# Kernel optimization log

Hardware: AMD Instinct MI355X
Metric: run time of the kernel (lower is better)

Reference implementation:

```python
import jax, jax.numpy as jnp
import numpy as np
import math

N = 8192
F_IN = 1024
F_OUT = 1024
MAX_ITER = 10


def whale_optimizer(positions, key, max_iter=MAX_ITER):
    """Vectorized whale optimization algorithm.

    Faithful to the original per-agent/per-dim update rules, but the agent
    loop is vectorized (on-device RNG, one parallel update per outer
    iteration); only the `max_iter` outer iterations stay sequential.
    positions: [N, D] float32.
    """
    n, d = positions.shape
    lower = jnp.min(positions)
    upper = jnp.max(positions)
    k0, loop_key = jax.random.split(key)
    leader = positions[jax.random.randint(k0, (), 0, n)]  # [D]

    def step(carry, it):
        pos, leader = carry
        itf = it.astype(jnp.float32)
        k = jax.random.fold_in(loop_key, it)
        k1, k2, k3, k4, k5, k6 = jax.random.split(k, 6)
        a = 2.0 - itf * (2.0 / max_iter)
        a2 = -1.0 + itf * (-1.0 / max_iter)
        r1 = jax.random.uniform(k1, (n, 1))
        r2 = jax.random.uniform(k2, (n, 1))
        A = 2.0 * a * r1 - a                       # [n,1]
        C = 2.0 * r2                               # [n,1]
        lp = (a2 - 1.0) * jax.random.uniform(k3, (n, 1)) + 1.0  # spiral param
        p = jax.random.uniform(k4, (n, 1))
        # random leader per (agent, dim), as in the original inner j-loop
        ridx = jax.random.randint(k5, (n, d), 0, n)
        x_rand = jnp.take_along_axis(pos, ridx, axis=0)         # [n,d]
        explore = jnp.abs(x_rand - A * jnp.abs(C * x_rand - pos))
        exploit = jnp.abs(leader - A * jnp.abs(C * leader - pos))
        spiral = jnp.abs(jnp.abs(leader - pos) * jnp.exp(lp) * jnp.cos(2.0 * jnp.pi * lp) + leader)
        new_pos = jnp.where(p < 0.5,
                            jnp.where(jnp.abs(A) >= 1.0, explore, exploit),
                            spiral)
        new_pos = jnp.clip(new_pos, lower, upper)
        new_leader = new_pos[jax.random.randint(k6, (), 0, n)]
        return (new_pos, new_leader), None

    (positions, _), _ = jax.lax.scan(step, (positions, leader), jnp.arange(max_iter))
    return positions


def setup_inputs() -> dict:
    key = jax.random.key(0)
    k1, k2, k3, k4 = jax.random.split(key, 4)
    stdv = 1.0 / math.sqrt(F_OUT)
    return {
        "input": jax.random.normal(k1, (N, F_IN), dtype=jnp.float32),
        "adj": jax.random.uniform(k2, (N, N), dtype=jnp.float32) * (1.0 / N),
        "h0": jax.random.normal(k3, (N, F_IN), dtype=jnp.float32),
        "weight": jax.random.uniform(k4, (F_IN, F_OUT), dtype=jnp.float32,
                                      minval=-stdv, maxval=stdv),
        "lamda": jnp.float32(0.5),
        "alpha": jnp.float32(0.1),
        "l": 1,
    }


def reference(input, adj, h0, weight, lamda, alpha, l):
    # variant=False, residual=False
    theta = jnp.log(lamda / l + 1.0)
    hi = adj @ input                                  # spmm(adj, input)
    support = (1.0 - alpha) * hi + alpha * h0
    r = support
    # original detaches support before the whale optimizer
    opt = whale_optimizer(jax.lax.stop_gradient(support), jax.random.key(42))
    output = theta * (opt @ weight) + (1.0 - theta) * r
    return output
```

## Files before the change

kernel.cpp:

```cpp
#include <hip/hip_runtime.h>
#include <hip/hip_bf16.h>
#include <stdint.h>
#include <math.h>

typedef uint32_t u32;
typedef __hip_bfloat16 bf16t;
typedef __attribute__((ext_vector_type(8))) short short8;
typedef __attribute__((ext_vector_type(4))) float f32x4;


__host__ __device__ __forceinline__ void tf2(u32 k0, u32 k1, u32 c0, u32 c1, u32& o0, u32& o1) {
  const u32 ks2 = k0 ^ k1 ^ 0x1BD11BDAu;
  u32 x0 = c0 + k0, x1 = c1 + k1;
#define TFROT(v,r) (((v)<<(r))|((v)>>(32-(r))))
#define TFR(r) { x0 += x1; x1 = TFROT(x1,r); x1 ^= x0; }
  TFR(13) TFR(15) TFR(26) TFR(6)   x0 += k1;  x1 += ks2 + 1u;
  TFR(17) TFR(29) TFR(16) TFR(24)  x0 += ks2; x1 += k0 + 2u;
  TFR(13) TFR(15) TFR(26) TFR(6)   x0 += k0;  x1 += k1 + 3u;
  TFR(17) TFR(29) TFR(16) TFR(24)  x0 += k1;  x1 += ks2 + 4u;
  TFR(13) TFR(15) TFR(26) TFR(6)   x0 += ks2; x1 += k0 + 5u;
#undef TFR
#undef TFROT
  o0 = x0; o1 = x1;
}

__device__ __forceinline__ float unif_row(u32 ka, u32 kb, int i) {
  u32 o0, o1;
  tf2(ka, kb, 0u, (u32)i, o0, o1);
  return __uint_as_float(0x3F800000u | ((o0 ^ o1) >> 9)) - 1.0f;
}

__device__ __forceinline__ int ridx_fn(u32 ka, u32 kb, u32 f) {
  u32 o0, o1; tf2(ka, kb, 0u, f, o0, o1); return (int)((o0 ^ o1) & 8191u);
}

static inline void split2(u32 ka, u32 kb, u32* kA, u32* kB) {
  u32 a0, a1, b0, b1;
  tf2(ka, kb, 0u, 0u, a0, a1);
  tf2(ka, kb, 0u, 1u, b0, b1);
  kA[0] = a0; kA[1] = a1; kB[0] = b0; kB[1] = b1;
}

static inline void split6(u32 ka, u32 kb, u32 out[6][2]) {
  for (u32 i = 0; i < 6; i++) { u32 o0, o1; tf2(ka, kb, 0u, i, o0, o1); out[i][0] = o0; out[i][1] = o1; }
}

static inline int scalar_randint8192(u32 ka, u32 kb) {
  u32 kA[2], kB[2];
  split2(ka, kb, kA, kB);
  u32 o0, o1;
  tf2(kB[0], kB[1], 0u, 0u, o0, o1);
  return (int)((o0 ^ o1) & 8191u);
}

__device__ __forceinline__ ushort f2bf(float f) {
  u32 u = __float_as_uint(f);
  u32 r = u + 0x7FFFu + ((u >> 16) & 1u);
  return (ushort)(r >> 16);
}

__global__ __launch_bounds__(256) void packb_k(const float* __restrict__ B, uint4* __restrict__ out, int K, int Nn) {
  const int idx = blockIdx.x * 256 + threadIdx.x;
  const int total = (K >> 3) * Nn;
  if (idx >= total) return;
  const int g = idx / Nn;
  const int n = idx - g * Nn;
  u32 wv[4];
#pragma unroll
  for (int j = 0; j < 4; j++) {
    const float f0 = B[(size_t)(g * 8 + 2 * j) * Nn + n];
    const float f1 = B[(size_t)(g * 8 + 2 * j + 1) * Nn + n];
    wv[j] = (u32)f2bf(f0) | ((u32)f2bf(f1) << 16);
  }
  uint4 o; o.x = wv[0]; o.y = wv[1]; o.z = wv[2]; o.w = wv[3];
  out[idx] = o;
}

__global__ __launch_bounds__(256) void minmax2_k(const float* __restrict__ part, int G, float* __restrict__ bnd) {
  __shared__ float slo[256], shi[256];
  const int tid = threadIdx.x;
  float lo = 3.4e38f, hi = -3.4e38f;
  for (int i = tid; i < G; i += 256) { lo = fminf(lo, part[i]); hi = fmaxf(hi, part[G + i]); }
  slo[tid] = lo; shi[tid] = hi; __syncthreads();
  for (int s = 128; s > 0; s >>= 1) {
    if (tid < s) { slo[tid] = fminf(slo[tid], slo[tid + s]); shi[tid] = fmaxf(shi[tid], shi[tid + s]); }
    __syncthreads();
  }
  if (tid == 0) { bnd[0] = slo[0]; bnd[1] = shi[0]; }
}

__device__ __forceinline__ void gld_lds16(const void* g, void* l) {
  __builtin_amdgcn_global_load_lds((const __attribute__((address_space(1))) void*)g,
                                   (__attribute__((address_space(3))) void*)l, 16, 0, 0);
}

template <int EPI, int AF32>
__global__ __launch_bounds__(512, 4) void gemm_k(
    const void* __restrict__ Araw, const bf16t* __restrict__ Bp,
    const float* __restrict__ aux, const float* __restrict__ sF,
    const int* __restrict__ sI, float* __restrict__ C,
    float* __restrict__ prt, int PG, int Nn, int K) {
  constexpr int APAD = 72;
  __shared__ __align__(16) bf16t As[2][128 * APAD];
  __shared__ __align__(16) bf16t Bs[2][128 * 64];
  const int tid = threadIdx.x;
  const int lane = tid & 63;
  const int wave = tid >> 6;
  const int bm = blockIdx.x & 63;
  const int bn = blockIdx.x >> 6;
  const int m0 = bm << 7, n0 = bn << 7;
  const int wm = (wave & 1) << 6;
  const int wn = (wave >> 1) << 5;

  f32x4 acc[4][2];
#pragma unroll
  for (int i = 0; i < 4; i++)
#pragma unroll
    for (int j = 0; j < 2; j++) acc[i][j] = (f32x4){0.f, 0.f, 0.f, 0.f};

  const float* Af = (const float*)Araw;
  const bf16t* Ab = (const bf16t*)Araw;
  const int u0 = tid, u1 = tid + 512;
  const int ar0 = u0 >> 3, ac0 = (u0 & 7) << 3;
  const int ar1 = u1 >> 3, ac1 = (u1 & 7) << 3;
  const bf16t* gB0 = Bp + ((size_t)(u0 >> 7) * Nn + n0 + (u0 & 127)) * 8;
  const bf16t* gB1 = Bp + ((size_t)(u1 >> 7) * Nn + n0 + (u1 & 127)) * 8;
  const size_t bstep = (size_t)Nn * 64;

  float4 a32[2][2];
  short8 a16[2];

  auto issueA = [&](int s) {
    if (AF32) {
      const float* p0 = Af + (size_t)(m0 + ar0) * K + (s << 6) + ac0;
      const float* p1 = Af + (size_t)(m0 + ar1) * K + (s << 6) + ac1;
      a32[0][0] = *(const float4*)p0; a32[0][1] = *(const float4*)(p0 + 4);
      a32[1][0] = *(const float4*)p1; a32[1][1] = *(const float4*)(p1 + 4);
    } else {
      a16[0] = *(const short8*)(Ab + (size_t)(m0 + ar0) * K + (s << 6) + ac0);
      a16[1] = *(const short8*)(Ab + (size_t)(m0 + ar1) * K + (s << 6) + ac1);
    }
  };
  auto writeA = [&](int buf) {
#pragma unroll
    for (int i = 0; i < 2; i++) {
      short8 v;
      if (AF32) {
#pragma unroll
        for (int e = 0; e < 4; e++) v[e] = (short)f2bf((&a32[i][0].x)[e]);
#pragma unroll
        for (int e = 0; e < 4; e++) v[4 + e] = (short)f2bf((&a32[i][1].x)[e]);
      } else {
        v = a16[i];
      }
      const int r = i ? ar1 : ar0, cc = i ? ac1 : ac0;
      *(short8*)(&As[buf][r * APAD + cc]) = v;
    }
  };
  auto stageB = [&](int s, int buf) {
    gld_lds16(gB0 + (size_t)s * bstep, &Bs[buf][u0 << 3]);
    gld_lds16(gB1 + (size_t)s * bstep, &Bs[buf][u1 << 3]);
  };

  issueA(0);
  stageB(0, 0);
  writeA(0);

  const int S = K >> 6;
  const int arow = lane & 15, aq = lane >> 4;
  for (int s = 0; s < S; ++s) {
    const int cur = s & 1;
    __syncthreads();
    const bool more = (s + 1 < S);
    if (more) { stageB(s + 1, cur ^ 1); issueA(s + 1); }
#pragma unroll
    for (int c = 0; c < 2; ++c) {
      short8 af[4], bfv[2];
#pragma unroll
      for (int mt = 0; mt < 4; mt++)
        af[mt] = *(const short8*)(&As[cur][(wm + mt * 16 + arow) * APAD + (c << 5) + (aq << 3)]);
#pragma unroll
      for (int nt = 0; nt < 2; nt++)
        bfv[nt] = *(const short8*)(&Bs[cur][(((c << 2) + aq) * 128 + wn + nt * 16 + arow) << 3]);
#pragma unroll
      for (int mt = 0; mt < 4; mt++)
#pragma unroll
        for (int nt = 0; nt < 2; nt++)
          acc[mt][nt] = __builtin_amdgcn_mfma_f32_16x16x32_bf16(af[mt], bfv[nt], acc[mt][nt], 0, 0, 0);
    }
    if (more) writeA(cur ^ 1);
  }

  float p1, p2;
  if (EPI == 1) { const float al = sF[0]; p1 = 1.0f - al; p2 = al; }
  else { const float th = logf(sF[0] / (float)sI[0] + 1.0f); p1 = th; p2 = 1.0f - th; }
  const int col = lane & 15, rq = lane >> 4;
  float vlo = 3.4e38f, vhi = -3.4e38f;
#pragma unroll
  for (int mt = 0; mt < 4; mt++)
#pragma unroll
    for (int nt = 0; nt < 2; nt++)
#pragma unroll
      for (int r = 0; r < 4; r++) {
        const int gm = m0 + wm + mt * 16 + (rq << 2) + r;
        const int gn = n0 + wn + nt * 16 + col;
        const size_t ix = (size_t)gm * Nn + gn;
        const float v = p1 * acc[mt][nt][r] + p2 * aux[ix];
        C[ix] = v;
        if (EPI == 1) { vlo = fminf(vlo, v); vhi = fmaxf(vhi, v); }
      }
  if (EPI == 1) {
    __syncthreads();
    float* red = (float*)&As[0][0];
    red[tid] = vlo; red[512 + tid] = vhi;
    __syncthreads();
    for (int s = 256; s > 0; s >>= 1) {
      if (tid < s) {
        red[tid] = fminf(red[tid], red[tid + s]);
        red[512 + tid] = fmaxf(red[512 + tid], red[512 + tid + s]);
      }
      __syncthreads();
    }
    if (tid == 0) { prt[blockIdx.x] = red[0]; prt[PG + blockIdx.x] = red[512]; }
  }
}

struct WA {
  u32 k1a, k1b, k2a, k2b, k3a, k3b, k4a, k4b, k5a, k5b;
  int ldr;
  float a, a2;
};

__global__ __launch_bounds__(256) void whale_k(
    const float* __restrict__ pinb, float* __restrict__ poutb,
    ushort* __restrict__ opt, const float* __restrict__ bnd, WA w) {
  const int row = blockIdx.x;
  const int tid = threadIdx.x;
  __shared__ float sh[4];
  if (tid < 4) {
    u32 ka, kb;
    if (tid == 0)      { ka = w.k1a; kb = w.k1b; }
    else if (tid == 1) { ka = w.k2a; kb = w.k2b; }
    else if (tid == 2) { ka = w.k3a; kb = w.k3b; }
    else               { ka = w.k4a; kb = w.k4b; }
    sh[tid] = unif_row(ka, kb, row);
  }
  __syncthreads();
  const float r1 = sh[0], r2 = sh[1], u3 = sh[2], p = sh[3];
  float t2 = (2.0f * w.a) * r1;
  asm volatile("" : "+v"(t2));
  const float A = t2 - w.a;
  const float Cc = 2.0f * r2;
  const float lo = bnd[0], hi = bnd[1];
  const float* pin = pinb + ((size_t)row << 10);
  const int j0 = tid << 2;
  float4 pv = *(const float4*)(pin + j0);
  float ov[4];
  const bool bp = (p < 0.5f);
  if (bp && (fabsf(A) >= 1.0f)) {
    const u32 fb = ((u32)row << 10) + (u32)j0;
#pragma unroll
    for (int e = 0; e < 4; e++) {
      const float pos = (&pv.x)[e];
      const int ri = ridx_fn(w.k5a, w.k5b, fb + (u32)e);
      const float xr = pinb[((size_t)ri << 10) + j0 + e];
      ov[e] = fabsf(xr - A * fabsf(Cc * xr - pos));
    }
  } else {
    const float* ldp = pinb + ((size_t)w.ldr << 10);
    float4 lv = *(const float4*)(ldp + j0);
    if (bp) {
#pragma unroll
      for (int e = 0; e < 4; e++) {
        const float pos = (&pv.x)[e], ld = (&lv.x)[e];
        ov[e] = fabsf(ld - A * fabsf(Cc * ld - pos));
      }
    } else {
      const float lp = (w.a2 - 1.0f) * u3 + 1.0f;
      const float s1 = expf(lp);
      const float s2 = cosf(6.2831855f * lp);
#pragma unroll
      for (int e = 0; e < 4; e++) {
        const float pos = (&pv.x)[e], ld = (&lv.x)[e];
        ov[e] = fabsf(fabsf(ld - pos) * s1 * s2 + ld);
      }
    }
  }
  float4 res;
#pragma unroll
  for (int e = 0; e < 4; e++) (&res.x)[e] = fminf(fmaxf(ov[e], lo), hi);
  *(float4*)(poutb + ((size_t)row << 10) + j0) = res;
  if (opt) {
    ushort4 o4;
    o4.x = f2bf(res.x); o4.y = f2bf(res.y); o4.z = f2bf(res.z); o4.w = f2bf(res.w);
    *(ushort4*)(opt + ((size_t)row << 10) + j0) = o4;
  }
}

extern "C" void kernel_launch(void* const* d_in, const int* in_sizes, int n_in,
                              void* d_out, int out_size, void* d_ws, size_t ws_size,
                              hipStream_t stream) {
  const float* inp = (const float*)d_in[0];
  const float* adj = (const float*)d_in[1];
  const float* h0  = (const float*)d_in[2];
  const float* wgt = (const float*)d_in[3];
  const float* lam = (const float*)d_in[4];
  const float* alp = (const float*)d_in[5];
  const int* lint  = (const int*)d_in[6];
  float* outp = (float*)d_out;

  char* ws = (char*)d_ws;
  float* P0   = (float*)(ws);
  float* P1   = (float*)(ws + 33554432);
  ushort* OPT = (ushort*)(ws + 67108864);
  bf16t* B1p  = (bf16t*)(ws + 134217728);
  bf16t* Wp   = (bf16t*)(ws + 150994944);
  float* SUP  = (float*)(ws + 153092096);
  float* PRT  = (float*)(ws + 186646528);
  float* BND  = (float*)(ws + 186662912);

  hipLaunchKernelGGL(packb_k, dim3(4096), dim3(256), 0, stream, inp, (uint4*)B1p, 8192, 1024);
  hipLaunchKernelGGL(packb_k, dim3(512), dim3(256), 0, stream, wgt, (uint4*)Wp, 1024, 1024);
  hipLaunchKernelGGL((gemm_k<1, 1>), dim3(512), dim3(512), 0, stream, (const void*)adj, B1p, h0, alp, lint,
                     SUP, PRT, 512, 1024, 8192);
  hipLaunchKernelGGL(minmax2_k, dim3(1), dim3(256), 0, stream, PRT, 512, BND);

  u32 k0k[2], lpk[2];
  split2(0u, 42u, k0k, lpk);
  int ldr = scalar_randint8192(k0k[0], k0k[1]);
  const float* cur = SUP;
  float* bufs[2] = {P0, P1};
  for (int it = 0; it < 10; ++it) {
    u32 ka, kb; tf2(lpk[0], lpk[1], 0u, (u32)it, ka, kb);
    u32 ks[6][2];
    split6(ka, kb, ks);
    u32 k5A[2], k5B[2];
    split2(ks[4][0], ks[4][1], k5A, k5B);
    WA w;
    w.k1a = ks[0][0]; w.k1b = ks[0][1];
    w.k2a = ks[1][0]; w.k2b = ks[1][1];
    w.k3a = ks[2][0]; w.k3b = ks[2][1];
    w.k4a = ks[3][0]; w.k4b = ks[3][1];
    w.k5a = k5B[0];   w.k5b = k5B[1];
    w.ldr = ldr;
    const float itf = (float)it;
    w.a = 2.0f - itf * 0.2f;
    w.a2 = -1.0f + itf * (-0.1f);
    float* nxt = bufs[it & 1];
    hipLaunchKernelGGL(whale_k, dim3(8192), dim3(256), 0, stream, cur, nxt,
                       (it == 9) ? OPT : (ushort*)nullptr, BND, w);
    cur = nxt;
    ldr = scalar_randint8192(ks[5][0], ks[5][1]);
  }
  hipLaunchKernelGGL((gemm_k<2, 0>), dim3(512), dim3(512), 0, stream, (const void*)OPT, Wp, SUP, lam, lint,
                     outp, (float*)nullptr, 0, 1024, 1024);
  (void)in_sizes; (void)n_in; (void)out_size; (void)ws_size;
}
```

Measured before the change: 863.7 us.

## Pre-pack adjacency to swizzled bf16 tiles and load A via direct-to-LDS

```diff
diff --git a/kernel.cpp b/kernel.cpp
--- a/kernel.cpp
+++ b/kernel.cpp
@@ -76,6 +76,28 @@
   out[idx] = o;
 }
 
+__global__ __launch_bounds__(256) void packa_k(const float* __restrict__ A, uint4* __restrict__ out,
+                                               int M, int K, int lgS) {
+  const int idx = blockIdx.x * 256 + threadIdx.x;
+  const int S = K >> 6;
+  const int total = ((M >> 7) * S) << 10;
+  if (idx >= total) return;
+  const int chunk = idx >> 10;
+  const int w = idx & 1023;
+  const int r = w >> 3, kq = w & 7;
+  const int cm = chunk >> lgS, s = chunk & (S - 1);
+  const float* src = A + (size_t)((cm << 7) + r) * K + (s << 6) + (kq << 3);
+  const float4 f0 = *(const float4*)src;
+  const float4 f1 = *(const float4*)(src + 4);
+  u32 wv[4];
+  wv[0] = (u32)f2bf(f0.x) | ((u32)f2bf(f0.y) << 16);
+  wv[1] = (u32)f2bf(f0.z) | ((u32)f2bf(f0.w) << 16);
+  wv[2] = (u32)f2bf(f1.x) | ((u32)f2bf(f1.y) << 16);
+  wv[3] = (u32)f2bf(f1.z) | ((u32)f2bf(f1.w) << 16);
+  uint4 o; o.x = wv[0]; o.y = wv[1]; o.z = wv[2]; o.w = wv[3];
+  out[((size_t)chunk << 10) + (r << 3) + (kq ^ (r & 7))] = o;
+}
+
 __global__ __launch_bounds__(256) void minmax2_k(const float* __restrict__ part, int G, float* __restrict__ bnd) {
   __shared__ float slo[256], shi[256];
   const int tid = threadIdx.x;
@@ -94,15 +116,14 @@
                                    (__attribute__((address_space(3))) void*)l, 16, 0, 0);
 }
 
-template <int EPI, int AF32>
-__global__ __launch_bounds__(512, 4) void gemm_k(
-    const void* __restrict__ Araw, const bf16t* __restrict__ Bp,
+template <int EPI>
+__global__ __launch_bounds__(256, 2) void gemm_k(
+    const bf16t* __restrict__ Ap, const bf16t* __restrict__ Bp,
     const float* __restrict__ aux, const float* __restrict__ sF,
     const int* __restrict__ sI, float* __restrict__ C,
     float* __restrict__ prt, int PG, int Nn, int K) {
-  constexpr int APAD = 72;
-  __shared__ __align__(16) bf16t As[2][128 * APAD];
-  __shared__ __align__(16) bf16t Bs[2][128 * 64];
+  __shared__ __align__(16) bf16t As[2][8192];
+  __shared__ __align__(16) bf16t Bs[2][8192];
   const int tid = threadIdx.x;
   const int lane = tid & 63;
   const int wave = tid >> 6;
@@ -110,85 +131,63 @@
   const int bn = blockIdx.x >> 6;
   const int m0 = bm << 7, n0 = bn << 7;
   const int wm = (wave & 1) << 6;
-  const int wn = (wave >> 1) << 5;
-
-  f32x4 acc[4][2];
+  const int wn = (wave >> 1) << 6;
+  const int S = K >> 6;
+
+  f32x4 acc[4][4];
 #pragma unroll
   for (int i = 0; i < 4; i++)
 #pragma unroll
-    for (int j = 0; j < 2; j++) acc[i][j] = (f32x4){0.f, 0.f, 0.f, 0.f};
-
-  const float* Af = (const float*)Araw;
-  const bf16t* Ab = (const bf16t*)Araw;
-  const int u0 = tid, u1 = tid + 512;
-  const int ar0 = u0 >> 3, ac0 = (u0 & 7) << 3;
-  const int ar1 = u1 >> 3, ac1 = (u1 & 7) << 3;
-  const bf16t* gB0 = Bp + ((size_t)(u0 >> 7) * Nn + n0 + (u0 & 127)) * 8;
-  const bf16t* gB1 = Bp + ((size_t)(u1 >> 7) * Nn + n0 + (u1 & 127)) * 8;
+    for (int j = 0; j < 4; j++) acc[i][j] = (f32x4){0.f, 0.f, 0.f, 0.f};
+
+  const bf16t* gA0 = Ap + (((size_t)bm * S) << 13);
+  const bf16t* gBj[4];
   const size_t bstep = (size_t)Nn * 64;
-
-  float4 a32[2][2];
-  short8 a16[2];
-
-  auto issueA = [&](int s) {
-    if (AF32) {
-      const float* p0 = Af + (size_t)(m0 + ar0) * K + (s << 6) + ac0;
-      const float* p1 = Af + (size_t)(m0 + ar1) * K + (s << 6) + ac1;
-      a32[0][0] = *(const float4*)p0; a32[0][1] = *(const float4*)(p0 + 4);
-      a32[1][0] = *(const float4*)p1; a32[1][1] = *(const float4*)(p1 + 4);
-    } else {
-      a16[0] = *(const short8*)(Ab + (size_t)(m0 + ar0) * K + (s << 6) + ac0);
-      a16[1] = *(const short8*)(Ab + (size_t)(m0 + ar1) * K + (s << 6) + ac1);
+#pragma unroll
+  for (int j = 0; j < 4; j++) {
+    const int u = tid + (j << 8);
+    gBj[j] = Bp + ((size_t)(u >> 7) * Nn + n0 + (u & 127)) * 8;
+  }
+  auto stage = [&](int s, int buf) {
+    const bf16t* a = gA0 + ((size_t)s << 13);
+#pragma unroll
+    for (int j = 0; j < 4; j++) {
+      const int u = tid + (j << 8);
+      gld_lds16(a + ((size_t)u << 3), &As[buf][u << 3]);
+    }
+#pragma unroll
+    for (int j = 0; j < 4; j++) {
+      const int u = tid + (j << 8);
+      gld_lds16(gBj[j] + (size_t)s * bstep, &Bs[buf][u << 3]);
     }
   };
-  auto writeA = [&](int buf) {
-#pragma unroll
-    for (int i = 0; i < 2; i++) {
-      short8 v;
-      if (AF32) {
-#pragma unroll
-        for (int e = 0; e < 4; e++) v[e] = (short)f2bf((&a32[i][0].x)[e]);
-#pragma unroll
-        for (int e = 0; e < 4; e++) v[4 + e] = (short)f2bf((&a32[i][1].x)[e]);
-      } else {
-        v = a16[i];
-      }
-      const int r = i ? ar1 : ar0, cc = i ? ac1 : ac0;
-      *(short8*)(&As[buf][r * APAD + cc]) = v;
-    }
-  };
-  auto stageB = [&](int s, int buf) {
-    gld_lds16(gB0 + (size_t)s * bstep, &Bs[buf][u0 << 3]);
-    gld_lds16(gB1 + (size_t)s * bstep, &Bs[buf][u1 << 3]);
-  };
-
-  issueA(0);
-  stageB(0, 0);
-  writeA(0);
-
-  const int S = K >> 6;
+
   const int arow = lane & 15, aq = lane >> 4;
+  const int abase = ((wm + arow) << 6) + ((aq ^ (arow & 7)) << 3);
+  const int bbase = ((aq << 7) + wn + arow) << 3;
+
+  stage(0, 0);
+
   for (int s = 0; s < S; ++s) {
     const int cur = s & 1;
     __syncthreads();
-    const bool more = (s + 1 < S);
-    if (more) { stageB(s + 1, cur ^ 1); issueA(s + 1); }
+    if (s + 1 < S) stage(s + 1, cur ^ 1);
 #pragma unroll
     for (int c = 0; c < 2; ++c) {
-      short8 af[4], bfv[2];
+      short8 af[4], bv[4];
+      const int ab = abase ^ (c << 5);
 #pragma unroll
       for (int mt = 0; mt < 4; mt++)
-        af[mt] = *(const short8*)(&As[cur][(wm + mt * 16 + arow) * APAD + (c << 5) + (aq << 3)]);
-#pragma unroll
-      for (int nt = 0; nt < 2; nt++)
-        bfv[nt] = *(const short8*)(&Bs[cur][(((c << 2) + aq) * 128 + wn + nt * 16 + arow) << 3]);
+        af[mt] = *(const short8*)(&As[cur][ab + mt * 1024]);
+#pragma unroll
+      for (int nt = 0; nt < 4; nt++)
+        bv[nt] = *(const short8*)(&Bs[cur][bbase + (c << 12) + (nt << 7)]);
 #pragma unroll
       for (int mt = 0; mt < 4; mt++)
 #pragma unroll
-        for (int nt = 0; nt < 2; nt++)
-          acc[mt][nt] = __builtin_amdgcn_mfma_f32_16x16x32_bf16(af[mt], bfv[nt], acc[mt][nt], 0, 0, 0);
-    }
-    if (more) writeA(cur ^ 1);
+        for (int nt = 0; nt < 4; nt++)
+          acc[mt][nt] = __builtin_amdgcn_mfma_f32_16x16x32_bf16(af[mt], bv[nt], acc[mt][nt], 0, 0, 0);
+    }
   }
 
   float p1, p2;
@@ -199,7 +198,7 @@
 #pragma unroll
   for (int mt = 0; mt < 4; mt++)
 #pragma unroll
-    for (int nt = 0; nt < 2; nt++)
+    for (int nt = 0; nt < 4; nt++)
 #pragma unroll
       for (int r = 0; r < 4; r++) {
         const int gm = m0 + wm + mt * 16 + (rq << 2) + r;
@@ -212,16 +211,16 @@
   if (EPI == 1) {
     __syncthreads();
     float* red = (float*)&As[0][0];
-    red[tid] = vlo; red[512 + tid] = vhi;
+    red[tid] = vlo; red[256 + tid] = vhi;
     __syncthreads();
-    for (int s = 256; s > 0; s >>= 1) {
+    for (int s = 128; s > 0; s >>= 1) {
       if (tid < s) {
         red[tid] = fminf(red[tid], red[tid + s]);
-        red[512 + tid] = fmaxf(red[512 + tid], red[512 + tid + s]);
+        red[256 + tid] = fmaxf(red[256 + tid], red[256 + tid + s]);
       }
       __syncthreads();
     }
-    if (tid == 0) { prt[blockIdx.x] = red[0]; prt[PG + blockIdx.x] = red[512]; }
+    if (tid == 0) { prt[blockIdx.x] = red[0]; prt[PG + blockIdx.x] = red[256]; }
   }
 }
 
@@ -293,7 +292,10 @@
   if (opt) {
     ushort4 o4;
     o4.x = f2bf(res.x); o4.y = f2bf(res.y); o4.z = f2bf(res.z); o4.w = f2bf(res.w);
-    *(ushort4*)(opt + ((size_t)row << 10) + j0) = o4;
+    const int rr = row & 127;
+    const size_t chunk = (size_t)((row >> 7) << 4) + (j0 >> 6);
+    ushort* dst = opt + (chunk << 13) + (rr << 6) + ((((j0 >> 3) & 7) ^ (rr & 7)) << 3) + (j0 & 7);
+    *(ushort4*)dst = o4;
   }
 }
 
@@ -307,9 +309,11 @@
   const float* lam = (const float*)d_in[4];
   const float* alp = (const float*)d_in[5];
   const int* lint  = (const int*)d_in[6];
+
   float* outp = (float*)d_out;
 
   char* ws = (char*)d_ws;
+  bf16t* Apk  = (bf16t*)(ws);
   float* P0   = (float*)(ws);
   float* P1   = (float*)(ws + 33554432);
   ushort* OPT = (ushort*)(ws + 67108864);
@@ -319,9 +323,10 @@
   float* PRT  = (float*)(ws + 186646528);
   float* BND  = (float*)(ws + 186662912);
 
+  hipLaunchKernelGGL(packa_k, dim3(32768), dim3(256), 0, stream, adj, (uint4*)Apk, 8192, 8192, 7);
   hipLaunchKernelGGL(packb_k, dim3(4096), dim3(256), 0, stream, inp, (uint4*)B1p, 8192, 1024);
   hipLaunchKernelGGL(packb_k, dim3(512), dim3(256), 0, stream, wgt, (uint4*)Wp, 1024, 1024);
-  hipLaunchKernelGGL((gemm_k<1, 1>), dim3(512), dim3(512), 0, stream, (const void*)adj, B1p, h0, alp, lint,
+  hipLaunchKernelGGL((gemm_k<1>), dim3(512), dim3(256), 0, stream, Apk, B1p, h0, alp, lint,
                      SUP, PRT, 512, 1024, 8192);
   hipLaunchKernelGGL(minmax2_k, dim3(1), dim3(256), 0, stream, PRT, 512, BND);
 
@@ -352,7 +357,7 @@
     cur = nxt;
     ldr = scalar_randint8192(ks[5][0], ks[5][1]);
   }
-  hipLaunchKernelGGL((gemm_k<2, 0>), dim3(512), dim3(512), 0, stream, (const void*)OPT, Wp, SUP, lam, lint,
+  hipLaunchKernelGGL((gemm_k<2>), dim3(512), dim3(256), 0, stream, (const bf16t*)OPT, Wp, SUP, lam, lint,
                      outp, (float*)nullptr, 0, 1024, 1024);
   (void)in_sizes; (void)n_in; (void)out_size; (void)ws_size;
 }
```

Result: no change. 856.6 us (-0.8%).
